# Kernel tuning notes

Measured on AMD Instinct MI355X. Metric: run time of the kernel, lower is better.

Reference implementation:

```python
import jax, jax.numpy as jnp
import numpy as np

D_MODEL = 1024
NUM_HEADS = 16
HEAD_DIM = D_MODEL // NUM_HEADS
B, S = 2, 2048


def setup_inputs() -> dict:
    key = jax.random.key(0)
    ks = jax.random.split(key, 5)
    x = jax.random.normal(ks[0], (B, S, D_MODEL), dtype=jnp.float32)
    # nn.Linear weights are [out_features, in_features]
    Wq = jax.random.normal(ks[1], (D_MODEL, D_MODEL), dtype=jnp.float32) / np.sqrt(D_MODEL)
    Wk = jax.random.normal(ks[2], (HEAD_DIM, D_MODEL), dtype=jnp.float32) / np.sqrt(D_MODEL)
    Wv = jax.random.normal(ks[3], (HEAD_DIM, D_MODEL), dtype=jnp.float32) / np.sqrt(D_MODEL)
    Wo = jax.random.normal(ks[4], (D_MODEL, D_MODEL), dtype=jnp.float32) / np.sqrt(D_MODEL)
    # causal mask, broadcastable to [B, H, S, S]; mask==0 positions get -inf
    mask = jnp.tril(jnp.ones((S, S), dtype=bool))[None, None]
    return {"x": x, "Wq": Wq, "Wk": Wk, "Wv": Wv, "Wo": Wo, "mask": mask}


def reference(x, Wq, Wk, Wv, Wo, mask):
    Bsz, Sl, D = x.shape
    H, hd = NUM_HEADS, HEAD_DIM
    q = (x @ Wq.T).reshape(Bsz, Sl, H, hd)          # [B,S,H,hd]
    k = x @ Wk.T                                    # [B,S,hd] (single shared KV head)
    v = x @ Wv.T                                    # [B,S,hd]
    scale = 1.0 / np.sqrt(hd).astype(np.float32)
    # scores: [B,H,S,S] — full O(n^2) matrix, as in the original module
    scores = jnp.einsum('bshd,btd->bhst', q, k) * scale
    scores = jnp.where(mask, scores, -jnp.inf)
    attn = jax.nn.softmax(scores, axis=-1)
    out = jnp.einsum('bhst,btd->bshd', attn, v).reshape(Bsz, Sl, D)
    return out @ Wo.T
```

## Files before the change

kernel.cpp:

```cpp
#include <hip/hip_runtime.h>
#include <hip/hip_bf16.h>
#include <math.h>

#define BB 2
#define SS 2048
#define DD 1024
#define NH 16
#define HD 64
#define MM (BB * SS)

#define BK 32

typedef __hip_bfloat16 bf16;
typedef __bf16 bf16_t;
typedef __attribute__((ext_vector_type(8))) __bf16 bf16x8;
typedef __attribute__((ext_vector_type(4))) __bf16 bf16x4;
typedef __attribute__((ext_vector_type(4))) float floatx4;

#define SCALEQ 0.18033688011112042f

__global__ void detect_dtype(const unsigned int* __restrict__ x, int* __restrict__ flag) {
    const int tid = threadIdx.x;
    int good = 0;
    for (int i = tid; i < 256; i += 64) {
        unsigned int bits = (x[i] & 0xFFFFu) << 16;
        float v = __uint_as_float(bits);
        float av = fabsf(v);
        if (av == 0.f || (av >= 9.5367431640625e-7f && av <= 64.f)) good++;
    }
#pragma unroll
    for (int s = 1; s < 64; s <<= 1) good += __shfl_xor(good, s);
    if (tid == 0) { flag[0] = (good >= 240) ? 0 : 1; flag[1] = 0; }
}

__device__ __forceinline__ void conv_seg(const void* __restrict__ in,
                                         bf16_t* __restrict__ out,
                                         int n, int f, int tid, int T) {
    if (f) {
        const float* p = (const float*)in;
        for (int i = tid * 8; i < n; i += T * 8) {
            float4 a = *(const float4*)(p + i);
            float4 b = *(const float4*)(p + i + 4);
            bf16x8 o;
            o[0] = (bf16_t)a.x; o[1] = (bf16_t)a.y; o[2] = (bf16_t)a.z; o[3] = (bf16_t)a.w;
            o[4] = (bf16_t)b.x; o[5] = (bf16_t)b.y; o[6] = (bf16_t)b.z; o[7] = (bf16_t)b.w;
            *(bf16x8*)(out + i) = o;
        }
    } else {
        const bf16_t* p = (const bf16_t*)in;
        for (int i = tid * 8; i < n; i += T * 8)
            *(bf16x8*)(out + i) = *(const bf16x8*)(p + i);
    }
}

__global__ __launch_bounds__(256) void conv_all(const void* __restrict__ x,
                                                const void* __restrict__ wq,
                                                const void* __restrict__ wk,
                                                const void* __restrict__ wv,
                                                const void* __restrict__ wo,
                                                bf16_t* __restrict__ xb,
                                                bf16_t* __restrict__ wqb,
                                                bf16_t* __restrict__ wkb,
                                                bf16_t* __restrict__ wvb,
                                                bf16_t* __restrict__ wob,
                                                const int* __restrict__ flag) {
    const int f = *flag;
    const int tid = blockIdx.x * blockDim.x + threadIdx.x;
    const int T = gridDim.x * blockDim.x;
    conv_seg(x, xb, MM * DD, f, tid, T);
    conv_seg(wq, wqb, DD * DD, f, tid, T);
    conv_seg(wk, wkb, HD * DD, f, tid, T);
    conv_seg(wv, wvb, HD * DD, f, tid, T);
    conv_seg(wo, wob, DD * DD, f, tid, T);
}

#define KP2 40

__global__ __launch_bounds__(512) void proj_qkv_b(const bf16_t* __restrict__ X,
                                                  const bf16_t* __restrict__ Wq,
                                                  const bf16_t* __restrict__ Wk,
                                                  const bf16_t* __restrict__ Wv,
                                                  bf16_t* __restrict__ QA,
                                                  bf16_t* __restrict__ Kp,
                                                  bf16_t* __restrict__ VpT) {
    __shared__ bf16_t As[128 * KP2];
    __shared__ bf16_t Bs[128 * KP2];

    const int tid = threadIdx.x;
    const int wave = tid >> 6, lane = tid & 63;
    const int lo = lane & 15, quad = lane >> 4;
    const int wr = wave >> 2, wc = wave & 3;
    const int cb = blockIdx.x;
    const int rowBase = blockIdx.y * 128;

    const int rS = tid >> 2;
    const int cS = (tid & 3) * 8;

    const bf16_t* arow = X + (size_t)(rowBase + rS) * DD + cS;
    const bf16_t* wrow;
    if (cb < 8)       wrow = Wq + (size_t)(cb * 128 + rS) * DD + cS;
    else if (rS < 64) wrow = Wk + (size_t)rS * DD + cS;
    else              wrow = Wv + (size_t)(rS - 64) * DD + cS;

    floatx4 acc[4][2];
#pragma unroll
    for (int i = 0; i < 4; i++)
#pragma unroll
        for (int j = 0; j < 2; j++) acc[i][j] = (floatx4){0.f, 0.f, 0.f, 0.f};

    bf16x8 aR0 = *(const bf16x8*)(arow);
    bf16x8 bR0 = *(const bf16x8*)(wrow);
    bf16x8 aR1 = *(const bf16x8*)(arow + BK);
    bf16x8 bR1 = *(const bf16x8*)(wrow + BK);

    for (int k0 = 0; k0 < DD; k0 += 2 * BK) {
        __syncthreads();
        *(bf16x8*)&As[rS * KP2 + cS] = aR0;
        *(bf16x8*)&Bs[rS * KP2 + cS] = bR0;
        __syncthreads();
        if (k0 + 2 * BK < DD) {
            aR0 = *(const bf16x8*)(arow + k0 + 2 * BK);
            bR0 = *(const bf16x8*)(wrow + k0 + 2 * BK);
        }
        {
            bf16x8 afr[4], bfr[2];
#pragma unroll
            for (int i = 0; i < 4; i++)
                afr[i] = *(const bf16x8*)&As[(wr * 64 + i * 16 + lo) * KP2 + quad * 8];
#pragma unroll
            for (int j = 0; j < 2; j++)
                bfr[j] = *(const bf16x8*)&Bs[(wc * 32 + j * 16 + lo) * KP2 + quad * 8];
#pragma unroll
            for (int i = 0; i < 4; i++)
#pragma unroll
                for (int j = 0; j < 2; j++)
                    acc[i][j] = __builtin_amdgcn_mfma_f32_16x16x32_bf16(afr[i], bfr[j], acc[i][j], 0, 0, 0);
        }
        __syncthreads();
        *(bf16x8*)&As[rS * KP2 + cS] = aR1;
        *(bf16x8*)&Bs[rS * KP2 + cS] = bR1;
        __syncthreads();
        if (k0 + 3 * BK < DD) {
            aR1 = *(const bf16x8*)(arow + k0 + 3 * BK);
            bR1 = *(const bf16x8*)(wrow + k0 + 3 * BK);
        }
        {
            bf16x8 afr[4], bfr[2];
#pragma unroll
            for (int i = 0; i < 4; i++)
                afr[i] = *(const bf16x8*)&As[(wr * 64 + i * 16 + lo) * KP2 + quad * 8];
#pragma unroll
            for (int j = 0; j < 2; j++)
                bfr[j] = *(const bf16x8*)&Bs[(wc * 32 + j * 16 + lo) * KP2 + quad * 8];
#pragma unroll
            for (int i = 0; i < 4; i++)
#pragma unroll
                for (int j = 0; j < 2; j++)
                    acc[i][j] = __builtin_amdgcn_mfma_f32_16x16x32_bf16(afr[i], bfr[j], acc[i][j], 0, 0, 0);
        }
    }

#pragma unroll
    for (int i = 0; i < 4; i++)
#pragma unroll
        for (int j = 0; j < 2; j++)
#pragma unroll
            for (int reg = 0; reg < 4; reg++) {
                int row = rowBase + wr * 64 + i * 16 + quad * 4 + reg;
                int c = wc * 32 + j * 16 + lo;
                float v = acc[i][j][reg];
                if (cb < 8) {
                    QA[(size_t)row * DD + cb * 128 + c] = (bf16_t)(v * SCALEQ);
                } else if (c < 64) {
                    Kp[(size_t)row * HD + c] = (bf16_t)v;
                } else {
                    VpT[((size_t)(row >> 11) * HD + (c - 64)) * SS + (row & (SS - 1))] = (bf16_t)v;
                }
            }
}

__global__ __launch_bounds__(512) void proj_o_b(const bf16_t* __restrict__ AO,
                                                const bf16_t* __restrict__ Wo,
                                                void* __restrict__ Cout,
                                                const int* __restrict__ flagOut) {
    const int fout = *flagOut;

    __shared__ bf16_t As[128 * KP2];
    __shared__ bf16_t Bs[128 * KP2];

    const int tid = threadIdx.x;
    const int wave = tid >> 6, lane = tid & 63;
    const int lo = lane & 15, quad = lane >> 4;
    const int wr = wave >> 2, wc = wave & 3;
    const int colBase = blockIdx.x * 128;
    const int rowBase = blockIdx.y * 128;

    const int rS = tid >> 2;
    const int cS = (tid & 3) * 8;

    const bf16_t* arow = AO + (size_t)(rowBase + rS) * DD + cS;
    const bf16_t* wrow = Wo + (size_t)(colBase + rS) * DD + cS;

    floatx4 acc[4][2];
#pragma unroll
    for (int i = 0; i < 4; i++)
#pragma unroll
        for (int j = 0; j < 2; j++) acc[i][j] = (floatx4){0.f, 0.f, 0.f, 0.f};

    bf16x8 aR0 = *(const bf16x8*)(arow);
    bf16x8 bR0 = *(const bf16x8*)(wrow);
    bf16x8 aR1 = *(const bf16x8*)(arow + BK);
    bf16x8 bR1 = *(const bf16x8*)(wrow + BK);

    for (int k0 = 0; k0 < DD; k0 += 2 * BK) {
        __syncthreads();
        *(bf16x8*)&As[rS * KP2 + cS] = aR0;
        *(bf16x8*)&Bs[rS * KP2 + cS] = bR0;
        __syncthreads();
        if (k0 + 2 * BK < DD) {
            aR0 = *(const bf16x8*)(arow + k0 + 2 * BK);
            bR0 = *(const bf16x8*)(wrow + k0 + 2 * BK);
        }
        {
            bf16x8 afr[4], bfr[2];
#pragma unroll
            for (int i = 0; i < 4; i++)
                afr[i] = *(const bf16x8*)&As[(wr * 64 + i * 16 + lo) * KP2 + quad * 8];
#pragma unroll
            for (int j = 0; j < 2; j++)
                bfr[j] = *(const bf16x8*)&Bs[(wc * 32 + j * 16 + lo) * KP2 + quad * 8];
#pragma unroll
            for (int i = 0; i < 4; i++)
#pragma unroll
                for (int j = 0; j < 2; j++)
                    acc[i][j] = __builtin_amdgcn_mfma_f32_16x16x32_bf16(afr[i], bfr[j], acc[i][j], 0, 0, 0);
        }
        __syncthreads();
        *(bf16x8*)&As[rS * KP2 + cS] = aR1;
        *(bf16x8*)&Bs[rS * KP2 + cS] = bR1;
        __syncthreads();
        if (k0 + 3 * BK < DD) {
            aR1 = *(const bf16x8*)(arow + k0 + 3 * BK);
            bR1 = *(const bf16x8*)(wrow + k0 + 3 * BK);
        }
        {
            bf16x8 afr[4], bfr[2];
#pragma unroll
            for (int i = 0; i < 4; i++)
                afr[i] = *(const bf16x8*)&As[(wr * 64 + i * 16 + lo) * KP2 + quad * 8];
#pragma unroll
            for (int j = 0; j < 2; j++)
                bfr[j] = *(const bf16x8*)&Bs[(wc * 32 + j * 16 + lo) * KP2 + quad * 8];
#pragma unroll
            for (int i = 0; i < 4; i++)
#pragma unroll
                for (int j = 0; j < 2; j++)
                    acc[i][j] = __builtin_amdgcn_mfma_f32_16x16x32_bf16(afr[i], bfr[j], acc[i][j], 0, 0, 0);
        }
    }

#pragma unroll
    for (int i = 0; i < 4; i++)
#pragma unroll
        for (int j = 0; j < 2; j++)
#pragma unroll
            for (int reg = 0; reg < 4; reg++) {
                int row = rowBase + wr * 64 + i * 16 + quad * 4 + reg;
                int col = colBase + wc * 32 + j * 16 + lo;
                size_t idx = (size_t)row * DD + col;
                if (fout) ((float*)Cout)[idx] = acc[i][j][reg];
                else      ((bf16_t*)Cout)[idx] = (bf16_t)acc[i][j][reg];
            }
}

#define KP 40

__device__ __forceinline__ bf16x4 cvt4(float4 v) {
    bf16x4 o;
    o[0] = (bf16_t)v.x; o[1] = (bf16_t)v.y; o[2] = (bf16_t)v.z; o[3] = (bf16_t)v.w;
    return o;
}

__global__ __launch_bounds__(256) void proj_qkv(const void* __restrict__ X,
                                                const void* __restrict__ Wq,
                                                const void* __restrict__ Wk,
                                                const void* __restrict__ Wv,
                                                bf16_t* __restrict__ QA,
                                                bf16_t* __restrict__ Kp,
                                                bf16_t* __restrict__ VpT,
                                                const int* __restrict__ flag) {
    const int f = *flag;

    __shared__ bf16_t As[128 * KP];
    __shared__ bf16_t Ws[64 * KP];

    const int tid = threadIdx.x;
    const int wave = tid >> 6, lane = tid & 63;
    const int lo = lane & 15, quad = lane >> 4;
    const int rb = wave * 32;
    const int cb = blockIdx.x;
    const int rowBase = blockIdx.y * 128;

    floatx4 acc[2][4];
#pragma unroll
    for (int i = 0; i < 2; i++)
#pragma unroll
        for (int j = 0; j < 4; j++) acc[i][j] = (floatx4){0.f, 0.f, 0.f, 0.f};

    if (f) {
        const int rA = tid >> 3, sg = tid & 7;
        const float* arow[4];
        const float* wrow[2];
#pragma unroll
        for (int p = 0; p < 4; p++)
            arow[p] = (const float*)X + (size_t)(rowBase + rA + 32 * p) * DD;
#pragma unroll
        for (int p = 0; p < 2; p++) {
            int row = rA + 32 * p;
            if (cb < 16)       wrow[p] = (const float*)Wq + (size_t)(cb * 64 + row) * DD;
            else if (cb == 16) wrow[p] = (const float*)Wk + (size_t)row * DD;
            else               wrow[p] = (const float*)Wv + (size_t)row * DD;
        }
        float4 aR[4], wR[2];
#pragma unroll
        for (int p = 0; p < 4; p++) aR[p] = *(const float4*)(arow[p] + sg * 4);
#pragma unroll
        for (int p = 0; p < 2; p++) wR[p] = *(const float4*)(wrow[p] + sg * 4);

        for (int k0 = 0; k0 < DD; k0 += BK) {
            __syncthreads();
#pragma unroll
            for (int p = 0; p < 4; p++)
                *(bf16x4*)&As[(rA + 32 * p) * KP + sg * 4] = cvt4(aR[p]);
#pragma unroll
            for (int p = 0; p < 2; p++)
                *(bf16x4*)&Ws[(rA + 32 * p) * KP + sg * 4] = cvt4(wR[p]);
            __syncthreads();
            if (k0 + BK < DD) {
#pragma unroll
                for (int p = 0; p < 4; p++) aR[p] = *(const float4*)(arow[p] + k0 + BK + sg * 4);
#pragma unroll
                for (int p = 0; p < 2; p++) wR[p] = *(const float4*)(wrow[p] + k0 + BK + sg * 4);
            }
            bf16x8 afr[2], bfr[4];
#pragma unroll
            for (int i = 0; i < 2; i++)
                afr[i] = *(const bf16x8*)&As[(rb + i * 16 + lo) * KP + quad * 8];
#pragma unroll
            for (int j = 0; j < 4; j++)
                bfr[j] = *(const bf16x8*)&Ws[(j * 16 + lo) * KP + quad * 8];
#pragma unroll
            for (int i = 0; i < 2; i++)
#pragma unroll
                for (int j = 0; j < 4; j++)
                    acc[i][j] = __builtin_amdgcn_mfma_f32_16x16x32_bf16(afr[i], bfr[j], acc[i][j], 0, 0, 0);
        }
    } else {
        const int rA = tid >> 2, sg = tid & 3;
        const bf16_t* arow[2];
        const bf16_t* wrow;
#pragma unroll
        for (int p = 0; p < 2; p++)
            arow[p] = (const bf16_t*)X + (size_t)(rowBase + rA + 64 * p) * DD;
        if (cb < 16)       wrow = (const bf16_t*)Wq + (size_t)(cb * 64 + rA) * DD;
        else if (cb == 16) wrow = (const bf16_t*)Wk + (size_t)rA * DD;
        else               wrow = (const bf16_t*)Wv + (size_t)rA * DD;
        bf16x8 aR[2], wR;
#pragma unroll
        for (int p = 0; p < 2; p++) aR[p] = *(const bf16x8*)(arow[p] + sg * 8);
        wR = *(const bf16x8*)(wrow + sg * 8);

        for (int k0 = 0; k0 < DD; k0 += BK) {
            __syncthreads();
#pragma unroll
            for (int p = 0; p < 2; p++)
                *(bf16x8*)&As[(rA + 64 * p) * KP + sg * 8] = aR[p];
            *(bf16x8*)&Ws[rA * KP + sg * 8] = wR;
            __syncthreads();
            if (k0 + BK < DD) {
#pragma unroll
                for (int p = 0; p < 2; p++) aR[p] = *(const bf16x8*)(arow[p] + k0 + BK + sg * 8);
                wR = *(const bf16x8*)(wrow + k0 + BK + sg * 8);
            }
            bf16x8 afr[2], bfr[4];
#pragma unroll
            for (int i = 0; i < 2; i++)
                afr[i] = *(const bf16x8*)&As[(rb + i * 16 + lo) * KP + quad * 8];
#pragma unroll
            for (int j = 0; j < 4; j++)
                bfr[j] = *(const bf16x8*)&Ws[(j * 16 + lo) * KP + quad * 8];
#pragma unroll
            for (int i = 0; i < 2; i++)
#pragma unroll
                for (int j = 0; j < 4; j++)
                    acc[i][j] = __builtin_amdgcn_mfma_f32_16x16x32_bf16(afr[i], bfr[j], acc[i][j], 0, 0, 0);
        }
    }

#pragma unroll
    for (int i = 0; i < 2; i++)
#pragma unroll
        for (int j = 0; j < 4; j++)
#pragma unroll
            for (int reg = 0; reg < 4; reg++) {
                int row = rowBase + rb + i * 16 + quad * 4 + reg;
                int col = j * 16 + lo;
                if (cb < 16) {
                    QA[(size_t)row * DD + cb * 64 + col] = (bf16_t)(acc[i][j][reg] * SCALEQ);
                } else if (cb == 16) {
                    Kp[(size_t)row * HD + col] = (bf16_t)acc[i][j][reg];
                } else {
                    VpT[((size_t)(row >> 11) * HD + col) * SS + (row & (SS - 1))] =
                        (bf16_t)acc[i][j][reg];
                }
            }
}

__global__ __launch_bounds__(256) void proj_o(const bf16_t* __restrict__ AO,
                                              const void* __restrict__ Wo,
                                              void* __restrict__ Cout,
                                              const int* __restrict__ flagW,
                                              const int* __restrict__ flagOut) {
    const int f = *flagW;
    const int fout = *flagOut;

    __shared__ bf16_t As[128 * KP];
    __shared__ bf16_t Ws[64 * KP];

    const int tid = threadIdx.x;
    const int wave = tid >> 6, lane = tid & 63;
    const int lo = lane & 15, quad = lane >> 4;
    const int rb = wave * 32;
    const int colBase = blockIdx.x * 64;
    const int rowBase = blockIdx.y * 128;

    floatx4 acc[2][4];
#pragma unroll
    for (int i = 0; i < 2; i++)
#pragma unroll
        for (int j = 0; j < 4; j++) acc[i][j] = (floatx4){0.f, 0.f, 0.f, 0.f};

    const int rA2 = tid >> 2, sgA = tid & 3;
    const bf16_t* arow[2] = {AO + (size_t)(rowBase + rA2) * DD,
                             AO + (size_t)(rowBase + rA2 + 64) * DD};
    bf16x8 aR[2];
#pragma unroll
    for (int p = 0; p < 2; p++) aR[p] = *(const bf16x8*)(arow[p] + sgA * 8);

    if (f) {
        const int rW = tid >> 3, sgW = tid & 7;
        const float* wrow[2];
#pragma unroll
        for (int p = 0; p < 2; p++)
            wrow[p] = (const float*)Wo + (size_t)(colBase + rW + 32 * p) * DD;
        float4 wR[2];
#pragma unroll
        for (int p = 0; p < 2; p++) wR[p] = *(const float4*)(wrow[p] + sgW * 4);

        for (int k0 = 0; k0 < DD; k0 += BK) {
            __syncthreads();
#pragma unroll
            for (int p = 0; p < 2; p++)
                *(bf16x8*)&As[(rA2 + 64 * p) * KP + sgA * 8] = aR[p];
#pragma unroll
            for (int p = 0; p < 2; p++)
                *(bf16x4*)&Ws[(rW + 32 * p) * KP + sgW * 4] = cvt4(wR[p]);
            __syncthreads();
            if (k0 + BK < DD) {
#pragma unroll
                for (int p = 0; p < 2; p++) aR[p] = *(const bf16x8*)(arow[p] + k0 + BK + sgA * 8);
#pragma unroll
                for (int p = 0; p < 2; p++) wR[p] = *(const float4*)(wrow[p] + k0 + BK + sgW * 4);
            }
            bf16x8 afr[2], bfr[4];
#pragma unroll
            for (int i = 0; i < 2; i++)
                afr[i] = *(const bf16x8*)&As[(rb + i * 16 + lo) * KP + quad * 8];
#pragma unroll
            for (int j = 0; j < 4; j++)
                bfr[j] = *(const bf16x8*)&Ws[(j * 16 + lo) * KP + quad * 8];
#pragma unroll
            for (int i = 0; i < 2; i++)
#pragma unroll
                for (int j = 0; j < 4; j++)
                    acc[i][j] = __builtin_amdgcn_mfma_f32_16x16x32_bf16(afr[i], bfr[j], acc[i][j], 0, 0, 0);
        }
    } else {
        const bf16_t* wrow = (const bf16_t*)Wo + (size_t)(colBase + rA2) * DD;
        bf16x8 wR = *(const bf16x8*)(wrow + sgA * 8);

        for (int k0 = 0; k0 < DD; k0 += BK) {
            __syncthreads();
#pragma unroll
            for (int p = 0; p < 2; p++)
                *(bf16x8*)&As[(rA2 + 64 * p) * KP + sgA * 8] = aR[p];
            *(bf16x8*)&Ws[rA2 * KP + sgA * 8] = wR;
            __syncthreads();
            if (k0 + BK < DD) {
#pragma unroll
                for (int p = 0; p < 2; p++) aR[p] = *(const bf16x8*)(arow[p] + k0 + BK + sgA * 8);
                wR = *(const bf16x8*)(wrow + k0 + BK + sgA * 8);
            }
            bf16x8 afr[2], bfr[4];
#pragma unroll
            for (int i = 0; i < 2; i++)
                afr[i] = *(const bf16x8*)&As[(rb + i * 16 + lo) * KP + quad * 8];
#pragma unroll
            for (int j = 0; j < 4; j++)
                bfr[j] = *(const bf16x8*)&Ws[(j * 16 + lo) * KP + quad * 8];
#pragma unroll
            for (int i = 0; i < 2; i++)
#pragma unroll
                for (int j = 0; j < 4; j++)
                    acc[i][j] = __builtin_amdgcn_mfma_f32_16x16x32_bf16(afr[i], bfr[j], acc[i][j], 0, 0, 0);
        }
    }

#pragma unroll
    for (int i = 0; i < 2; i++)
#pragma unroll
        for (int j = 0; j < 4; j++)
#pragma unroll
            for (int reg = 0; reg < 4; reg++) {
                int row = rowBase + rb + i * 16 + quad * 4 + reg;
                int col = colBase + j * 16 + lo;
                size_t idx = (size_t)row * DD + col;
                if (fout) ((float*)Cout)[idx] = acc[i][j][reg];
                else      ((bf16_t*)Cout)[idx] = (bf16_t)acc[i][j][reg];
            }
}

#define PSTR 40
#define DMTHR 8.0f

__global__ __launch_bounds__(512, 4) void attn_mfma(const bf16_t* Q,
                                                    const bf16_t* __restrict__ K,
                                                    const bf16_t* __restrict__ Vt,
                                                    bf16_t* O) {
    const int h = blockIdx.y, b = blockIdx.z;
    const int tid = threadIdx.x;
    const int wq = tid >> 6, lane = tid & 63;
    const int lo = lane & 15, quad = lane >> 4;
    const int x = blockIdx.x;

    const int nA = x + 1;
    int na = 1, bestc = 0x7fffffff;
#pragma unroll
    for (int a = 1; a <= 7; ++a) {
        int cA = (nA + a - 1) / a;
        int cB = (65 - nA + (7 - a)) / (8 - a);
        int c = cA > cB ? cA : cB;
        if (c < bestc) { bestc = c; na = a; }
    }
    int qt, pos, gs;
    if (wq < na) { qt = x;      pos = wq;      gs = na; }
    else         { qt = 63 - x; pos = wq - na; gs = 8 - na; }
    const int q0 = qt * 32;
    const int n = qt + 1;
    const int itS = (n * pos) / gs;
    const int itE = (n * (pos + 1)) / gs;

    __shared__ __align__(16) char smem[4 * 32 * 64 * 4];
    __shared__ float MrgML[4][2][2][16];
    bf16_t* Pw = (bf16_t*)smem + wq * (32 * PSTR);
    float (*MrgO)[32 * 64] = (float (*)[32 * 64])smem;

    bf16x8 qf[2][2];
#pragma unroll
    for (int s = 0; s < 2; s++)
#pragma unroll
        for (int hf = 0; hf < 2; hf++)
            qf[s][hf] = *(const bf16x8*)(Q + ((size_t)(b * SS + q0 + s * 16 + lo)) * DD +
                                         h * HD + hf * 32 + quad * 8);

    floatx4 Oacc[2][4];
    float m_i[2], l_ln[2];
#pragma unroll
    for (int s = 0; s < 2; s++) {
#pragma unroll
        for (int dt = 0; dt < 4; dt++) Oacc[s][dt] = (floatx4){0.f, 0.f, 0.f, 0.f};
        m_i[s] = -1e30f; l_ln[s] = 0.f;
    }

    const bf16_t* Kb = K + (size_t)b * SS * HD;
    const bf16_t* Vb = Vt + (size_t)b * HD * SS;

    if (itS < itE) {
        bf16x8 kf[2][2];
#pragma unroll
        for (int kt = 0; kt < 2; kt++)
#pragma unroll
            for (int hf = 0; hf < 2; hf++)
                kf[kt][hf] = *(const bf16x8*)(Kb + (size_t)(itS * 32 + kt * 16 + lo) * HD +
                                              hf * 32 + quad * 8);

        for (int it = itS; it < itE; it++) {
            const int t0 = it * 32;

            bf16x8 vf[4];
#pragma unroll
            for (int dt = 0; dt < 4; dt++)
                vf[dt] = *(const bf16x8*)(Vb + (size_t)(dt * 16 + lo) * SS + t0 + quad * 8);

            bf16x8 kn[2][2];
            if (it + 1 < itE) {
#pragma unroll
                for (int kt = 0; kt < 2; kt++)
#pragma unroll
                    for (int hf = 0; hf < 2; hf++)
                        kn[kt][hf] = *(const bf16x8*)(Kb + (size_t)(t0 + 32 + kt * 16 + lo) * HD +
                                                      hf * 32 + quad * 8);
            }

            floatx4 st[2][2];
#pragma unroll
            for (int s = 0; s < 2; s++)
#pragma unroll
                for (int kt = 0; kt < 2; kt++) {
                    floatx4 z = (floatx4){0.f, 0.f, 0.f, 0.f};
                    z = __builtin_amdgcn_mfma_f32_16x16x32_bf16(kf[kt][0], qf[s][0], z, 0, 0, 0);
                    z = __builtin_amdgcn_mfma_f32_16x16x32_bf16(kf[kt][1], qf[s][1], z, 0, 0, 0);
                    st[s][kt] = z;
                }

            if (it == qt) {
#pragma unroll
                for (int s = 0; s < 2; s++) {
                    int q = q0 + s * 16 + lo;
#pragma unroll
                    for (int kt = 0; kt < 2; kt++)
#pragma unroll
                        for (int reg = 0; reg < 4; reg++)
                            if (t0 + kt * 16 + quad * 4 + reg > q) st[s][kt][reg] = -1e30f;
                }
            }

#pragma unroll
            for (int s = 0; s < 2; s++) {
                float lm = fmaxf(fmaxf(fmaxf(st[s][0][0], st[s][0][1]), fmaxf(st[s][0][2], st[s][0][3])),
                                 fmaxf(fmaxf(st[s][1][0], st[s][1][1]), fmaxf(st[s][1][2], st[s][1][3])));
                if (__any(lm > m_i[s] + DMTHR)) {
                    float mx = fmaxf(lm, __shfl_xor(lm, 16));
                    mx = fmaxf(mx, __shfl_xor(mx, 32));
                    float mn = fmaxf(m_i[s], mx);
                    float al = exp2f(m_i[s] - mn);
                    m_i[s] = mn;
                    l_ln[s] *= al;
#pragma unroll
                    for (int dt = 0; dt < 4; dt++) Oacc[s][dt] *= al;
                }
                float p[2][4];
#pragma unroll
                for (int kt = 0; kt < 2; kt++)
#pragma unroll
                    for (int reg = 0; reg < 4; reg++)
                        p[kt][reg] = exp2f(st[s][kt][reg] - m_i[s]);
                l_ln[s] += ((p[0][0] + p[0][1]) + (p[0][2] + p[0][3])) +
                           ((p[1][0] + p[1][1]) + (p[1][2] + p[1][3]));
#pragma unroll
                for (int kt = 0; kt < 2; kt++) {
                    bf16x4 pk;
#pragma unroll
                    for (int reg = 0; reg < 4; reg++) pk[reg] = (bf16_t)p[kt][reg];
                    *(bf16x4*)&Pw[(s * 16 + lo) * PSTR + kt * 16 + quad * 4] = pk;
                }
            }

            asm volatile("s_waitcnt lgkmcnt(0)" ::: "memory");

            bf16x8 pb[2];
#pragma unroll
            for (int s = 0; s < 2; s++)
                pb[s] = *(const bf16x8*)&Pw[(s * 16 + lo) * PSTR + quad * 8];
#pragma unroll
            for (int s = 0; s < 2; s++)
#pragma unroll
                for (int dt = 0; dt < 4; dt++)
                    Oacc[s][dt] = __builtin_amdgcn_mfma_f32_16x16x32_bf16(vf[dt], pb[s], Oacc[s][dt], 0, 0, 0);

#pragma unroll
            for (int kt = 0; kt < 2; kt++)
#pragma unroll
                for (int hf = 0; hf < 2; hf++) kf[kt][hf] = kn[kt][hf];
        }
    }

    float l_i[2];
#pragma unroll
    for (int s = 0; s < 2; s++) {
        float l = l_ln[s];
        l += __shfl_xor(l, 16);
        l += __shfl_xor(l, 32);
        l_i[s] = l;
    }

    for (int step = 1; step < 8; step <<= 1) {
        const bool pub = (pos & (2 * step - 1)) == step;
        const bool cmb = ((pos & (2 * step - 1)) == 0) && (pos + step < gs);
        __syncthreads();
        if (pub) {
            float* Ob = MrgO[wq >> 1];
#pragma unroll
            for (int s = 0; s < 2; s++) {
#pragma unroll
                for (int dt = 0; dt < 4; dt++)
#pragma unroll
                    for (int reg = 0; reg < 4; reg++)
                        Ob[(s * 16 + dt * 4 + reg) * 64 + lane] = Oacc[s][dt][reg];
                if (quad == 0) {
                    MrgML[wq >> 1][s][0][lo] = m_i[s];
                    MrgML[wq >> 1][s][1][lo] = l_i[s];
                }
            }
        }
        __syncthreads();
        if (cmb) {
            const int bu = (wq + step) >> 1;
            const float* Ob = MrgO[bu];
#pragma unroll
            for (int s = 0; s < 2; s++) {
                float m1 = MrgML[bu][s][0][lo];
                float l1 = MrgML[bu][s][1][lo];
                float mm = fmaxf(m_i[s], m1);
                float a0 = exp2f(m_i[s] - mm);
                float a1 = exp2f(m1 - mm);
                m_i[s] = mm;
                l_i[s] = l_i[s] * a0 + l1 * a1;
#pragma unroll
                for (int dt = 0; dt < 4; dt++)
#pragma unroll
                    for (int reg = 0; reg < 4; reg++)
                        Oacc[s][dt][reg] = Oacc[s][dt][reg] * a0 +
                                           Ob[(s * 16 + dt * 4 + reg) * 64 + lane] * a1;
            }
        }
    }

    if (pos == 0) {
#pragma unroll
        for (int s = 0; s < 2; s++) {
            float linv = 1.f / l_i[s];
            bf16_t* Orow = O + ((size_t)(b * SS + q0 + s * 16 + lo)) * DD + h * HD;
#pragma unroll
            for (int dt = 0; dt < 4; dt++) {
                bf16x4 ov;
#pragma unroll
                for (int reg = 0; reg < 4; reg++)
                    ov[reg] = (bf16_t)(Oacc[s][dt][reg] * linv);
                *(bf16x4*)&Orow[dt * 16 + quad * 4] = ov;
            }
        }
    }
}

extern "C" void kernel_launch(void* const* d_in, const int* in_sizes, int n_in,
                              void* d_out, int out_size, void* d_ws, size_t ws_size,
                              hipStream_t stream) {
    const void* x  = d_in[0];
    const void* Wq = d_in[1];
    const void* Wk = d_in[2];
    const void* Wv = d_in[3];
    const void* Wo = d_in[4];

    char* ws = (char*)d_ws;
    int* flag = (int*)ws;
    bf16_t* QA  = (bf16_t*)(ws + 256);
    bf16_t* Kp  = QA + (size_t)MM * DD;
    bf16_t* VpT = Kp + (size_t)MM * HD;
    bf16_t* Xb  = VpT + (size_t)BB * HD * SS;
    bf16_t* Wqb = Xb + (size_t)MM * DD;
    bf16_t* Wkb = Wqb + (size_t)DD * DD;
    bf16_t* Wvb = Wkb + (size_t)HD * DD;
    bf16_t* Wob = Wvb + (size_t)HD * DD;
    size_t need = (size_t)((char*)(Wob + (size_t)DD * DD) - ws);

    detect_dtype<<<1, 64, 0, stream>>>((const unsigned int*)x, flag);

    if (ws_size >= need) {
        conv_all<<<dim3(1024), dim3(256), 0, stream>>>(x, Wq, Wk, Wv, Wo,
                                                       Xb, Wqb, Wkb, Wvb, Wob, flag);
        proj_qkv_b<<<dim3(9, MM / 128), dim3(512), 0, stream>>>(Xb, Wqb, Wkb, Wvb,
                                                                QA, Kp, VpT);
        attn_mfma<<<dim3(32, NH, BB), dim3(512), 0, stream>>>(QA, Kp, VpT, QA);
        proj_o_b<<<dim3(8, MM / 128), dim3(512), 0, stream>>>(QA, Wob, d_out, flag);
    } else {
        proj_qkv<<<dim3(18, MM / 128), dim3(256), 0, stream>>>(x, Wq, Wk, Wv,
                                                               QA, Kp, VpT, flag);
        attn_mfma<<<dim3(32, NH, BB), dim3(512), 0, stream>>>(QA, Kp, VpT, QA);
        proj_o<<<dim3(16, MM / 128), dim3(256), 0, stream>>>(QA, Wo, d_out,
                                                             flag, flag);
    }
}
```

Before: 209.7 us.

## Use direct global-to-LDS loads with double buffering and XOR swizzle in projection GEMMs

Replaces the register-staged loads in the QKV and output projection GEMMs with global_load_lds, which writes 16-byte chunks straight into shared memory. Two shared buffers now alternate, so the next K tile loads while the current one is multiplied, and each step needs one barrier instead of two. The padded row stride is replaced by an XOR swizzle on the column chunk to avoid LDS bank conflicts. The loop relies on the barrier covering completion of the asynchronous LDS loads, and it adds a prologue and doubles the shared-memory footprint.

```diff
diff --git a/kernel.cpp b/kernel.cpp
--- a/kernel.cpp
+++ b/kernel.cpp
@@ -10,6 +10,7 @@
 #define MM (BB * SS)
 
 #define BK 32
+#define NT (DD / BK)
 
 typedef __hip_bfloat16 bf16;
 typedef __bf16 bf16_t;
@@ -18,6 +19,13 @@
 typedef __attribute__((ext_vector_type(4))) float floatx4;
 
 #define SCALEQ 0.18033688011112042f
+
+__device__ __forceinline__ void gload16(const bf16_t* g, bf16_t* l) {
+    __builtin_amdgcn_global_load_lds(
+        (const __attribute__((address_space(1))) unsigned int*)g,
+        (__attribute__((address_space(3))) unsigned int*)l,
+        16, 0, 0);
+}
 
 __global__ void detect_dtype(const unsigned int* __restrict__ x, int* __restrict__ flag) {
     const int tid = threadIdx.x;
@@ -74,8 +82,6 @@
     conv_seg(wo, wob, DD * DD, f, tid, T);
 }
 
-#define KP2 40
-
 __global__ __launch_bounds__(512) void proj_qkv_b(const bf16_t* __restrict__ X,
                                                   const bf16_t* __restrict__ Wq,
                                                   const bf16_t* __restrict__ Wk,
@@ -83,24 +89,25 @@
                                                   bf16_t* __restrict__ QA,
                                                   bf16_t* __restrict__ Kp,
                                                   bf16_t* __restrict__ VpT) {
-    __shared__ bf16_t As[128 * KP2];
-    __shared__ bf16_t Bs[128 * KP2];
+    __shared__ bf16_t As[2][128 * BK];
+    __shared__ bf16_t Bs[2][128 * BK];
 
     const int tid = threadIdx.x;
     const int wave = tid >> 6, lane = tid & 63;
     const int lo = lane & 15, quad = lane >> 4;
+    const int qsw = quad ^ (lo & 3);
     const int wr = wave >> 2, wc = wave & 3;
     const int cb = blockIdx.x;
     const int rowBase = blockIdx.y * 128;
 
     const int rS = tid >> 2;
-    const int cS = (tid & 3) * 8;
-
-    const bf16_t* arow = X + (size_t)(rowBase + rS) * DD + cS;
+    const int gsw = (((tid & 3) ^ (rS & 3)) * 8);
+
+    const bf16_t* arow = X + (size_t)(rowBase + rS) * DD + gsw;
     const bf16_t* wrow;
-    if (cb < 8)       wrow = Wq + (size_t)(cb * 128 + rS) * DD + cS;
-    else if (rS < 64) wrow = Wk + (size_t)rS * DD + cS;
-    else              wrow = Wv + (size_t)(rS - 64) * DD + cS;
+    if (cb < 8)       wrow = Wq + (size_t)(cb * 128 + rS) * DD + gsw;
+    else if (rS < 64) wrow = Wk + (size_t)rS * DD + gsw;
+    else              wrow = Wv + (size_t)(rS - 64) * DD + gsw;
 
     floatx4 acc[4][2];
 #pragma unroll
@@ -108,56 +115,31 @@
 #pragma unroll
         for (int j = 0; j < 2; j++) acc[i][j] = (floatx4){0.f, 0.f, 0.f, 0.f};
 
-    bf16x8 aR0 = *(const bf16x8*)(arow);
-    bf16x8 bR0 = *(const bf16x8*)(wrow);
-    bf16x8 aR1 = *(const bf16x8*)(arow + BK);
-    bf16x8 bR1 = *(const bf16x8*)(wrow + BK);
-
-    for (int k0 = 0; k0 < DD; k0 += 2 * BK) {
+    gload16(arow, &As[0][tid * 8]);
+    gload16(wrow, &Bs[0][tid * 8]);
+    __syncthreads();
+
+    int cur = 0;
+    for (int t = 0; t < NT; t++) {
+        if (t + 1 < NT) {
+            const int kn = (t + 1) * BK;
+            gload16(arow + kn, &As[cur ^ 1][tid * 8]);
+            gload16(wrow + kn, &Bs[cur ^ 1][tid * 8]);
+        }
+        bf16x8 afr[4], bfr[2];
+#pragma unroll
+        for (int i = 0; i < 4; i++)
+            afr[i] = *(const bf16x8*)&As[cur][(wr * 64 + i * 16 + lo) * BK + qsw * 8];
+#pragma unroll
+        for (int j = 0; j < 2; j++)
+            bfr[j] = *(const bf16x8*)&Bs[cur][(wc * 32 + j * 16 + lo) * BK + qsw * 8];
+#pragma unroll
+        for (int i = 0; i < 4; i++)
+#pragma unroll
+            for (int j = 0; j < 2; j++)
+                acc[i][j] = __builtin_amdgcn_mfma_f32_16x16x32_bf16(afr[i], bfr[j], acc[i][j], 0, 0, 0);
         __syncthreads();
-        *(bf16x8*)&As[rS * KP2 + cS] = aR0;
-        *(bf16x8*)&Bs[rS * KP2 + cS] = bR0;
-        __syncthreads();
-        if (k0 + 2 * BK < DD) {
-            aR0 = *(const bf16x8*)(arow + k0 + 2 * BK);
-            bR0 = *(const bf16x8*)(wrow + k0 + 2 * BK);
-        }
-        {
-            bf16x8 afr[4], bfr[2];
-#pragma unroll
-            for (int i = 0; i < 4; i++)
-                afr[i] = *(const bf16x8*)&As[(wr * 64 + i * 16 + lo) * KP2 + quad * 8];
-#pragma unroll
-            for (int j = 0; j < 2; j++)
-                bfr[j] = *(const bf16x8*)&Bs[(wc * 32 + j * 16 + lo) * KP2 + quad * 8];
-#pragma unroll
-            for (int i = 0; i < 4; i++)
-#pragma unroll
-                for (int j = 0; j < 2; j++)
-                    acc[i][j] = __builtin_amdgcn_mfma_f32_16x16x32_bf16(afr[i], bfr[j], acc[i][j], 0, 0, 0);
-        }
-        __syncthreads();
-        *(bf16x8*)&As[rS * KP2 + cS] = aR1;
-        *(bf16x8*)&Bs[rS * KP2 + cS] = bR1;
-        __syncthreads();
-        if (k0 + 3 * BK < DD) {
-            aR1 = *(const bf16x8*)(arow + k0 + 3 * BK);
-            bR1 = *(const bf16x8*)(wrow + k0 + 3 * BK);
-        }
-        {
-            bf16x8 afr[4], bfr[2];
-#pragma unroll
-            for (int i = 0; i < 4; i++)
-                afr[i] = *(const bf16x8*)&As[(wr * 64 + i * 16 + lo) * KP2 + quad * 8];
-#pragma unroll
-            for (int j = 0; j < 2; j++)
-                bfr[j] = *(const bf16x8*)&Bs[(wc * 32 + j * 16 + lo) * KP2 + quad * 8];
-#pragma unroll
-            for (int i = 0; i < 4; i++)
-#pragma unroll
-                for (int j = 0; j < 2; j++)
-                    acc[i][j] = __builtin_amdgcn_mfma_f32_16x16x32_bf16(afr[i], bfr[j], acc[i][j], 0, 0, 0);
-        }
+        cur ^= 1;
     }
 
 #pragma unroll
@@ -185,21 +167,22 @@
                                                 const int* __restrict__ flagOut) {
     const int fout = *flagOut;
 
-    __shared__ bf16_t As[128 * KP2];
-    __shared__ bf16_t Bs[128 * KP2];
+    __shared__ bf16_t As[2][128 * BK];
+    __shared__ bf16_t Bs[2][128 * BK];
 
     const int tid = threadIdx.x;
     const int wave = tid >> 6, lane = tid & 63;
     const int lo = lane & 15, quad = lane >> 4;
+    const int qsw = quad ^ (lo & 3);
     const int wr = wave >> 2, wc = wave & 3;
     const int colBase = blockIdx.x * 128;
     const int rowBase = blockIdx.y * 128;
 
     const int rS = tid >> 2;
-    const int cS = (tid & 3) * 8;
-
-    const bf16_t* arow = AO + (size_t)(rowBase + rS) * DD + cS;
-    const bf16_t* wrow = Wo + (size_t)(colBase + rS) * DD + cS;
+    const int gsw = (((tid & 3) ^ (rS & 3)) * 8);
+
+    const bf16_t* arow = AO + (size_t)(rowBase + rS) * DD + gsw;
+    const bf16_t* wrow = Wo + (size_t)(colBase + rS) * DD + gsw;
 
     floatx4 acc[4][2];
 #pragma unroll
@@ -207,56 +190,31 @@
 #pragma unroll
         for (int j = 0; j < 2; j++) acc[i][j] = (floatx4){0.f, 0.f, 0.f, 0.f};
 
-    bf16x8 aR0 = *(const bf16x8*)(arow);
-    bf16x8 bR0 = *(const bf16x8*)(wrow);
-    bf16x8 aR1 = *(const bf16x8*)(arow + BK);
-    bf16x8 bR1 = *(const bf16x8*)(wrow + BK);
-
-    for (int k0 = 0; k0 < DD; k0 += 2 * BK) {
+    gload16(arow, &As[0][tid * 8]);
+    gload16(wrow, &Bs[0][tid * 8]);
+    __syncthreads();
+
+    int cur = 0;
+    for (int t = 0; t < NT; t++) {
+        if (t + 1 < NT) {
+            const int kn = (t + 1) * BK;
+            gload16(arow + kn, &As[cur ^ 1][tid * 8]);
+            gload16(wrow + kn, &Bs[cur ^ 1][tid * 8]);
+        }
+        bf16x8 afr[4], bfr[2];
+#pragma unroll
+        for (int i = 0; i < 4; i++)
+            afr[i] = *(const bf16x8*)&As[cur][(wr * 64 + i * 16 + lo) * BK + qsw * 8];
+#pragma unroll
+        for (int j = 0; j < 2; j++)
+            bfr[j] = *(const bf16x8*)&Bs[cur][(wc * 32 + j * 16 + lo) * BK + qsw * 8];
+#pragma unroll
+        for (int i = 0; i < 4; i++)
+#pragma unroll
+            for (int j = 0; j < 2; j++)
+                acc[i][j] = __builtin_amdgcn_mfma_f32_16x16x32_bf16(afr[i], bfr[j], acc[i][j], 0, 0, 0);
         __syncthreads();
-        *(bf16x8*)&As[rS * KP2 + cS] = aR0;
-        *(bf16x8*)&Bs[rS * KP2 + cS] = bR0;
-        __syncthreads();
-        if (k0 + 2 * BK < DD) {
-            aR0 = *(const bf16x8*)(arow + k0 + 2 * BK);
-            bR0 = *(const bf16x8*)(wrow + k0 + 2 * BK);
-        }
-        {
-            bf16x8 afr[4], bfr[2];
-#pragma unroll
-            for (int i = 0; i < 4; i++)
-                afr[i] = *(const bf16x8*)&As[(wr * 64 + i * 16 + lo) * KP2 + quad * 8];
-#pragma unroll
-            for (int j = 0; j < 2; j++)
-                bfr[j] = *(const bf16x8*)&Bs[(wc * 32 + j * 16 + lo) * KP2 + quad * 8];
-#pragma unroll
-            for (int i = 0; i < 4; i++)
-#pragma unroll
-                for (int j = 0; j < 2; j++)
-                    acc[i][j] = __builtin_amdgcn_mfma_f32_16x16x32_bf16(afr[i], bfr[j], acc[i][j], 0, 0, 0);
-        }
-        __syncthreads();
-        *(bf16x8*)&As[rS * KP2 + cS] = aR1;
-        *(bf16x8*)&Bs[rS * KP2 + cS] = bR1;
-        __syncthreads();
-        if (k0 + 3 * BK < DD) {
-            aR1 = *(const bf16x8*)(arow + k0 + 3 * BK);
-            bR1 = *(const bf16x8*)(wrow + k0 + 3 * BK);
-        }
-        {
-            bf16x8 afr[4], bfr[2];
-#pragma unroll
-            for (int i = 0; i < 4; i++)
-                afr[i] = *(const bf16x8*)&As[(wr * 64 + i * 16 + lo) * KP2 + quad * 8];
-#pragma unroll
-            for (int j = 0; j < 2; j++)
-                bfr[j] = *(const bf16x8*)&Bs[(wc * 32 + j * 16 + lo) * KP2 + quad * 8];
-#pragma unroll
-            for (int i = 0; i < 4; i++)
-#pragma unroll
-                for (int j = 0; j < 2; j++)
-                    acc[i][j] = __builtin_amdgcn_mfma_f32_16x16x32_bf16(afr[i], bfr[j], acc[i][j], 0, 0, 0);
-        }
+        cur ^= 1;
     }
 
 #pragma unroll
```

New measurement: 221.1 us. +5.4%, slower.
